# Optimization experiments

Measured on AMD Instinct MI355X. Metric: run time of the kernel, lower is better.

Reference implementation:

```python
import jax, jax.numpy as jnp
import numpy as np

NUM_HEADS = 16
HEAD_DIM = 64
D_MODEL = NUM_HEADS * HEAD_DIM  # 1024
B, L = 512, 64


def setup_inputs() -> dict:
    key = jax.random.key(0)
    ks = jax.random.split(key, 6)
    s = 1.0 / np.sqrt(D_MODEL)
    x = jax.random.normal(ks[0], (B, L, D_MODEL), dtype=jnp.float32)
    bias = jax.random.normal(ks[1], (1, NUM_HEADS, L, L), dtype=jnp.float32)
    Wq = jax.random.normal(ks[2], (D_MODEL, NUM_HEADS * HEAD_DIM), dtype=jnp.float32) * s
    Wk = jax.random.normal(ks[3], (D_MODEL, NUM_HEADS * HEAD_DIM), dtype=jnp.float32) * s
    Wv = jax.random.normal(ks[4], (D_MODEL, NUM_HEADS * HEAD_DIM), dtype=jnp.float32) * s
    Wo = jax.random.normal(ks[5], (NUM_HEADS * HEAD_DIM, D_MODEL), dtype=jnp.float32) * s
    return {"x": x, "bias": bias, "Wq": Wq, "Wk": Wk, "Wv": Wv, "Wo": Wo}


def reference(x, bias, Wq, Wk, Wv, Wo):
    Bsz, Ls, D = x.shape
    H, Dh = NUM_HEADS, HEAD_DIM
    # QKV projections (no bias), reshape to [B, H, L, Dh]
    q = (x @ Wq).reshape(Bsz, Ls, H, Dh).transpose(0, 2, 1, 3)
    k = (x @ Wk).reshape(Bsz, Ls, H, Dh).transpose(0, 2, 1, 3)
    v = (x @ Wv).reshape(Bsz, Ls, H, Dh).transpose(0, 2, 1, 3)
    scale = jnp.sqrt(jnp.float32(Dh))
    # [B, H, L, L]
    attn_logits = jnp.einsum('bhqd,bhkd->bhqk', q, k) / scale + bias
    attn_weights = jax.nn.softmax(attn_logits, axis=-1)
    # weighted sum -> [B, L, H*Dh]
    out = jnp.einsum('bhqk,bhkd->bhqd', attn_weights, v)
    out = out.transpose(0, 2, 1, 3).reshape(Bsz, Ls, H * Dh)
    return out @ Wo
```

## Files before the change

### kernel.cpp

```cpp
#include <hip/hip_runtime.h>
#include <hip/hip_bf16.h>
#include <stdint.h>

__device__ inline float bf2f(ushort u) {
    union { uint32_t u; float f; } v; v.u = ((uint32_t)u) << 16; return v.f;
}
__device__ inline ushort f2bf(float f) {
    union { float f; uint32_t u; } v; v.f = f;
    uint32_t u = v.u;
    uint32_t r = (u + 0x7fffu + ((u >> 16) & 1u)) >> 16;
    return (ushort)r;
}
__device__ inline uint32_t pk2bf(uint32_t flo, uint32_t fhi) {
    uint32_t lo = (flo + 0x7fffu + ((flo >> 16) & 1u)) >> 16;
    uint32_t hi = (fhi + 0x7fffu + ((fhi >> 16) & 1u)) >> 16;
    return lo | (hi << 16);
}

typedef __attribute__((ext_vector_type(8))) short bf16x8;
typedef __attribute__((ext_vector_type(4))) float f32x4;

__device__ inline void gload_lds16(const ushort* g, ushort* l) {
    __builtin_amdgcn_global_load_lds(
        (const __attribute__((address_space(1))) void*)g,
        (__attribute__((address_space(3))) void*)l, 16, 0, 0);
}

__global__ void transpose1024(const float* __restrict__ Wq, const float* __restrict__ Wk,
                              const float* __restrict__ Wv, const float* __restrict__ Wo,
                              ushort* __restrict__ WqT, ushort* __restrict__ WkT,
                              ushort* __restrict__ WvT, ushort* __restrict__ WoT) {
    const float* in; ushort* out;
    switch (blockIdx.z) {
        case 0: in = Wq; out = WqT; break;
        case 1: in = Wk; out = WkT; break;
        case 2: in = Wv; out = WvT; break;
        default: in = Wo; out = WoT; break;
    }
    __shared__ ushort tile[64][65];
    const int t = threadIdx.x;
    const int c = t & 63, rq = t >> 6;
    const int bx = blockIdx.x * 64, by = blockIdx.y * 64;
#pragma unroll
    for (int i = 0; i < 16; ++i) {
        int r = i * 4 + rq;
        tile[r][c] = f2bf(in[(size_t)(by + r) * 1024 + bx + c]);
    }
    __syncthreads();
#pragma unroll
    for (int i = 0; i < 16; ++i) {
        int r = i * 4 + rq;
        out[(size_t)(bx + r) * 1024 + by + c] = tile[c][r];
    }
}

__global__ __launch_bounds__(256)
void cast_bf16(const float* __restrict__ in, ushort* __restrict__ out, size_t n8) {
    size_t i = (size_t)blockIdx.x * blockDim.x + threadIdx.x;
    const size_t stride = (size_t)gridDim.x * blockDim.x;
    for (; i < n8; i += stride) {
        const uint4 lo = *(const uint4*)&in[i * 8];
        const uint4 hi = *(const uint4*)&in[i * 8 + 4];
        uint4 o;
        o.x = pk2bf(lo.x, lo.y); o.y = pk2bf(lo.z, lo.w);
        o.z = pk2bf(hi.x, hi.y); o.w = pk2bf(hi.z, hi.w);
        *(uint4*)&out[i * 8] = o;
    }
}

template <bool C_F32>
__global__ __launch_bounds__(512, 2)
void gemm256(const ushort* __restrict__ A, int lda, const ushort* __restrict__ Bt,
             void* __restrict__ C_, int M, int N, int K, int cm, int cn) {
    __shared__ __attribute__((aligned(16))) ushort lds[65536];
    const int t = threadIdx.x;
    const int lane = t & 63, wave = t >> 6;
    const int wm = wave >> 2, wn = wave & 3;
    const int quad = lane >> 4, l16 = lane & 15;

    const int gx = N >> 8;
    const int wg0 = blockIdx.y * gridDim.x + blockIdx.x;
    const int xcd = wg0 & 7, loc = wg0 >> 3;
    const int ncx = gx / cn;
    const int crow = xcd / ncx, ccol = xcd % ncx;
    int mt, nt;
    if (cn <= cm) { nt = ccol * cn + loc % cn; mt = crow * cm + loc / cn; }
    else          { mt = crow * cm + loc % cm; nt = ccol * cn + loc / cm; }
    const int m0 = mt << 8, n0 = nt << 8;

    const f32x4 zero = {0.f, 0.f, 0.f, 0.f};
    f32x4 acc[8][4];
#pragma unroll
    for (int i = 0; i < 8; ++i)
#pragma unroll
        for (int j = 0; j < 4; ++j) acc[i][j] = zero;

    auto STAGE = [&](const ushort* __restrict__ src, int ldb, int rc0, int kcol,
                     int regio, int buf) {
        ushort* l = &lds[buf * 32768 + regio];
#pragma unroll
        for (int j = 0; j < 2; ++j) {
            const int g = j * 512 + t;
            const int r = g >> 2;
            const int cg = (((g & 3) ^ ((r >> 1) & 3)) * 8);
            gload_lds16(&src[(size_t)(rc0 + r) * ldb + kcol + cg],
                        &l[(j * 512 + wave * 64) * 8]);
        }
    };
    auto LOFF = [&](int R) { return R * 32 + (quad ^ ((R >> 1) & 3)) * 8; };

    const int NT = K >> 6;
    STAGE(A, lda, m0, 0, 0, 0);
    STAGE(Bt, K, n0, 0, 16384, 0);
    STAGE(A, lda, m0, 32, 8192, 0);
    STAGE(Bt, K, n0, 32, 24576, 0);
    asm volatile("s_waitcnt vmcnt(4)" ::: "memory");
    __builtin_amdgcn_s_barrier();

    int cur = 0;
    for (int kt = 0; kt < NT; ++kt) {
        const bool nx = kt + 1 < NT;
        const int kn = (kt + 1) << 6;
        const ushort* la0 = &lds[cur * 32768];
        const ushort* lb0 = &lds[cur * 32768 + 16384];
        const ushort* la1 = la0 + 8192;
        const ushort* lb1 = lb0 + 8192;
        bf16x8 af[4], bf[4];

#pragma unroll
        for (int i = 0; i < 4; ++i) {
            af[i] = *(const bf16x8*)&la0[LOFF(wm * 128 + i * 16 + l16)];
            bf[i] = *(const bf16x8*)&lb0[LOFF(wn * 64 + i * 16 + l16)];
        }
        if (nx) STAGE(A, lda, m0, kn, 0, cur ^ 1);
        __builtin_amdgcn_sched_barrier(0);
        __builtin_amdgcn_s_barrier();
        asm volatile("s_waitcnt lgkmcnt(0)" ::: "memory");
        __builtin_amdgcn_sched_barrier(0);
        __builtin_amdgcn_s_setprio(1);
#pragma unroll
        for (int i = 0; i < 4; ++i)
#pragma unroll
            for (int n = 0; n < 4; ++n)
                acc[i][n] = __builtin_amdgcn_mfma_f32_16x16x32_bf16(af[i], bf[n], acc[i][n], 0, 0, 0);
        __builtin_amdgcn_s_setprio(0);
        __builtin_amdgcn_sched_barrier(0);
        __builtin_amdgcn_s_barrier();

#pragma unroll
        for (int i = 0; i < 4; ++i)
            af[i] = *(const bf16x8*)&la0[LOFF(wm * 128 + (i + 4) * 16 + l16)];
        if (nx) STAGE(Bt, K, n0, kn, 16384, cur ^ 1);
        __builtin_amdgcn_sched_barrier(0);
        __builtin_amdgcn_s_barrier();
        asm volatile("s_waitcnt lgkmcnt(0)" ::: "memory");
        __builtin_amdgcn_sched_barrier(0);
        __builtin_amdgcn_s_setprio(1);
#pragma unroll
        for (int i = 0; i < 4; ++i)
#pragma unroll
            for (int n = 0; n < 4; ++n)
                acc[i + 4][n] = __builtin_amdgcn_mfma_f32_16x16x32_bf16(af[i], bf[n], acc[i + 4][n], 0, 0, 0);
        __builtin_amdgcn_s_setprio(0);
        if (nx) asm volatile("s_waitcnt vmcnt(4)" ::: "memory");
        else    asm volatile("s_waitcnt vmcnt(0)" ::: "memory");
        __builtin_amdgcn_sched_barrier(0);
        __builtin_amdgcn_s_barrier();

#pragma unroll
        for (int i = 0; i < 4; ++i) {
            af[i] = *(const bf16x8*)&la1[LOFF(wm * 128 + i * 16 + l16)];
            bf[i] = *(const bf16x8*)&lb1[LOFF(wn * 64 + i * 16 + l16)];
        }
        if (nx) STAGE(A, lda, m0, kn + 32, 8192, cur ^ 1);
        __builtin_amdgcn_sched_barrier(0);
        __builtin_amdgcn_s_barrier();
        asm volatile("s_waitcnt lgkmcnt(0)" ::: "memory");
        __builtin_amdgcn_sched_barrier(0);
        __builtin_amdgcn_s_setprio(1);
#pragma unroll
        for (int i = 0; i < 4; ++i)
#pragma unroll
            for (int n = 0; n < 4; ++n)
                acc[i][n] = __builtin_amdgcn_mfma_f32_16x16x32_bf16(af[i], bf[n], acc[i][n], 0, 0, 0);
        __builtin_amdgcn_s_setprio(0);
        __builtin_amdgcn_sched_barrier(0);
        __builtin_amdgcn_s_barrier();

#pragma unroll
        for (int i = 0; i < 4; ++i)
            af[i] = *(const bf16x8*)&la1[LOFF(wm * 128 + (i + 4) * 16 + l16)];
        if (nx) STAGE(Bt, K, n0, kn + 32, 24576, cur ^ 1);
        __builtin_amdgcn_sched_barrier(0);
        __builtin_amdgcn_s_barrier();
        asm volatile("s_waitcnt lgkmcnt(0)" ::: "memory");
        __builtin_amdgcn_sched_barrier(0);
        __builtin_amdgcn_s_setprio(1);
#pragma unroll
        for (int i = 0; i < 4; ++i)
#pragma unroll
            for (int n = 0; n < 4; ++n)
                acc[i + 4][n] = __builtin_amdgcn_mfma_f32_16x16x32_bf16(af[i], bf[n], acc[i + 4][n], 0, 0, 0);
        __builtin_amdgcn_s_setprio(0);
        if (nx) asm volatile("s_waitcnt vmcnt(4)" ::: "memory");
        __builtin_amdgcn_sched_barrier(0);
        __builtin_amdgcn_s_barrier();

        cur ^= 1;
    }

#pragma unroll
    for (int mt2 = 0; mt2 < 8; ++mt2)
#pragma unroll
        for (int nt2 = 0; nt2 < 4; ++nt2)
#pragma unroll
            for (int r4 = 0; r4 < 4; ++r4) {
                const int row = m0 + wm * 128 + mt2 * 16 + quad * 4 + r4;
                const int col = n0 + wn * 64 + nt2 * 16 + l16;
                if (C_F32) ((float*)C_)[(size_t)row * N + col] = acc[mt2][nt2][r4];
                else       ((ushort*)C_)[(size_t)row * N + col] = f2bf(acc[mt2][nt2][r4]);
            }
}

__global__ __launch_bounds__(256)
void attn_mfma(ushort* __restrict__ QK, const ushort* __restrict__ Vt,
               const float* __restrict__ bias, int CROWS) {
    const int t = threadIdx.x;
    const int lane = t & 63, wave = t >> 6;
    const int quad = lane >> 4, l16 = lane & 15;
    const int b = blockIdx.x >> 4, h = blockIdx.x & 15;
    const int SQK = 2048;
    const size_t qbase = (size_t)b * 64 * SQK + (size_t)h * 64;
    const size_t kbase = qbase + 1024;
    const size_t vbase = (size_t)(h * 64) * CROWS + (size_t)b * 64;

    __shared__ __attribute__((aligned(16))) ushort Pl[4 * 16 * 72];

    bf16x8 qf[2];
#pragma unroll
    for (int ks = 0; ks < 2; ++ks)
        qf[ks] = *(const bf16x8*)&QK[qbase + (size_t)(wave * 16 + l16) * SQK + ks * 32 + quad * 8];

    const f32x4 zero = {0.f, 0.f, 0.f, 0.f};
    f32x4 s[4];
#pragma unroll
    for (int nt = 0; nt < 4; ++nt) s[nt] = zero;
#pragma unroll
    for (int nt = 0; nt < 4; ++nt)
#pragma unroll
        for (int ks = 0; ks < 2; ++ks) {
            bf16x8 kf = *(const bf16x8*)&QK[kbase + (size_t)(nt * 16 + l16) * SQK + ks * 32 + quad * 8];
            s[nt] = __builtin_amdgcn_mfma_f32_16x16x32_bf16(qf[ks], kf, s[nt], 0, 0, 0);
        }

    const int q0 = wave * 16 + quad * 4;
    float p[4][4];
#pragma unroll
    for (int nt = 0; nt < 4; ++nt)
#pragma unroll
        for (int r4 = 0; r4 < 4; ++r4)
            p[nt][r4] = s[nt][r4] * 0.125f +
                        bias[(size_t)(h * 64 + q0 + r4) * 64 + nt * 16 + l16];

    float rinv[4];
#pragma unroll
    for (int r4 = 0; r4 < 4; ++r4) {
        float m = fmaxf(fmaxf(p[0][r4], p[1][r4]), fmaxf(p[2][r4], p[3][r4]));
        m = fmaxf(m, __shfl_xor(m, 1));
        m = fmaxf(m, __shfl_xor(m, 2));
        m = fmaxf(m, __shfl_xor(m, 4));
        m = fmaxf(m, __shfl_xor(m, 8));
#pragma unroll
        for (int nt = 0; nt < 4; ++nt) p[nt][r4] = __expf(p[nt][r4] - m);
        float sum = p[0][r4] + p[1][r4] + p[2][r4] + p[3][r4];
        sum += __shfl_xor(sum, 1);
        sum += __shfl_xor(sum, 2);
        sum += __shfl_xor(sum, 4);
        sum += __shfl_xor(sum, 8);
        rinv[r4] = 1.f / sum;
    }

#pragma unroll
    for (int nt = 0; nt < 4; ++nt)
#pragma unroll
        for (int r4 = 0; r4 < 4; ++r4)
            Pl[(wave * 16 + quad * 4 + r4) * 72 + nt * 16 + l16] = f2bf(p[nt][r4]);
    __syncthreads();

    bf16x8 pa[2];
#pragma unroll
    for (int ks = 0; ks < 2; ++ks)
        pa[ks] = *(const bf16x8*)&Pl[(wave * 16 + l16) * 72 + ks * 32 + quad * 8];
    f32x4 o[4];
#pragma unroll
    for (int nt = 0; nt < 4; ++nt) o[nt] = zero;
#pragma unroll
    for (int nt = 0; nt < 4; ++nt)
#pragma unroll
        for (int ks = 0; ks < 2; ++ks) {
            bf16x8 vf = *(const bf16x8*)&Vt[vbase + (size_t)(nt * 16 + l16) * CROWS + ks * 32 + quad * 8];
            o[nt] = __builtin_amdgcn_mfma_f32_16x16x32_bf16(pa[ks], vf, o[nt], 0, 0, 0);
        }

#pragma unroll
    for (int nt = 0; nt < 4; ++nt)
#pragma unroll
        for (int r4 = 0; r4 < 4; ++r4)
            QK[qbase + (size_t)(q0 + r4) * SQK + nt * 16 + l16] = f2bf(o[nt][r4] * rinv[r4]);
}

extern "C" void kernel_launch(void* const* d_in, const int* in_sizes, int n_in,
                              void* d_out, int out_size, void* d_ws, size_t ws_size,
                              hipStream_t stream) {
    const float* x    = (const float*)d_in[0];
    const float* bias = (const float*)d_in[1];
    const float* Wq   = (const float*)d_in[2];
    const float* Wk   = (const float*)d_in[3];
    const float* Wv   = (const float*)d_in[4];
    const float* Wo   = (const float*)d_in[5];
    float* out = (float*)d_out;

    const size_t D = 1024;
    const size_t WB = 4 * D * D * 2;

    int CHUNK_B = 128;
    if (ws_size >= WB + (size_t)512 * 64 * 6144)      CHUNK_B = 512;
    else if (ws_size >= WB + (size_t)256 * 64 * 6144) CHUNK_B = 256;
    const int NCHUNK = 512 / CHUNK_B;
    const size_t CROWS = (size_t)CHUNK_B * 64;
    const size_t CELEM = CROWS * D;

    ushort* WqT = (ushort*)d_ws;
    ushort* WkT = WqT + D * D;
    ushort* WvT = WkT + D * D;
    ushort* WoT = WvT + D * D;
    ushort* QKc = WoT + D * D;
    ushort* Vtc = QKc + CROWS * 2048;

    transpose1024<<<dim3(16, 16, 4), 256, 0, stream>>>(Wq, Wk, Wv, Wo, WqT, WkT, WvT, WoT);

    for (int c = 0; c < NCHUNK; ++c) {
        const float* xc = x + (size_t)c * CELEM;
        float* outc = out + (size_t)c * CELEM;
        ushort* Xc = (ushort*)outc;
        cast_bf16<<<2048, 256, 0, stream>>>(xc, Xc, CELEM / 8);
        gemm256<false><<<dim3(8, CROWS / 256), 512, 0, stream>>>(
            Xc, 1024, WqT, QKc, (int)CROWS, 2048, 1024,
            (int)(CROWS / 256 / 4), 4);
        gemm256<false><<<dim3(CROWS / 256, 4), 512, 0, stream>>>(
            WvT, 1024, Xc, Vtc, 1024, (int)CROWS, 1024,
            4, (int)(CROWS / 256 / 8));
        attn_mfma<<<CHUNK_B * 16, 256, 0, stream>>>(QKc, Vtc, bias, (int)CROWS);
        gemm256<true><<<dim3(4, CROWS / 256), 512, 0, stream>>>(
            QKc, 2048, WoT, outc, (int)CROWS, 1024, 1024,
            (int)(CROWS / 256 / 4), 2);
    }
}
```

Measured before the change: 617.4 us.

## Make GEMM kernel persistent over consecutive tiles with cross-tile prefetch

The GEMM kernel now loops over T consecutive output tiles per workgroup, with a grid sized to 256 workgroups. It prefetches the next tile's first K slab during the current tile's last iteration and writes the epilogue inline. This hides the per-tile prologue and launch tail, but it drops the XCD-aware tile swizzle. That can hurt L2 locality, because consecutive tiles in a row-major walk share A rows but use different B columns.

Measured after the change: 649.2 us. +5.1%, slower.

```diff
diff --git a/kernel.cpp b/kernel.cpp
--- a/kernel.cpp
+++ b/kernel.cpp
@@ -71,22 +71,14 @@
 template <bool C_F32>
 __global__ __launch_bounds__(512, 2)
 void gemm256(const ushort* __restrict__ A, int lda, const ushort* __restrict__ Bt,
-             void* __restrict__ C_, int M, int N, int K, int cm, int cn) {
+             void* __restrict__ C_, int M, int N, int K, int T) {
     __shared__ __attribute__((aligned(16))) ushort lds[65536];
     const int t = threadIdx.x;
     const int lane = t & 63, wave = t >> 6;
     const int wm = wave >> 2, wn = wave & 3;
     const int quad = lane >> 4, l16 = lane & 15;
-
     const int gx = N >> 8;
-    const int wg0 = blockIdx.y * gridDim.x + blockIdx.x;
-    const int xcd = wg0 & 7, loc = wg0 >> 3;
-    const int ncx = gx / cn;
-    const int crow = xcd / ncx, ccol = xcd % ncx;
-    int mt, nt;
-    if (cn <= cm) { nt = ccol * cn + loc % cn; mt = crow * cm + loc / cn; }
-    else          { mt = crow * cm + loc % cm; nt = ccol * cn + loc / cm; }
-    const int m0 = mt << 8, n0 = nt << 8;
+    const int wg = blockIdx.x;
 
     const f32x4 zero = {0.f, 0.f, 0.f, 0.f};
     f32x4 acc[8][4];
@@ -110,17 +102,27 @@
     auto LOFF = [&](int R) { return R * 32 + (quad ^ ((R >> 1) & 3)) * 8; };
 
     const int NT = K >> 6;
-    STAGE(A, lda, m0, 0, 0, 0);
-    STAGE(Bt, K, n0, 0, 16384, 0);
-    STAGE(A, lda, m0, 32, 8192, 0);
-    STAGE(Bt, K, n0, 32, 24576, 0);
+    const int GEND = T * NT;
+
+    int tidc = wg * T;
+    int mC = (tidc / gx) << 8, nC = (tidc % gx) << 8;
+
+    STAGE(A, lda, mC, 0, 0, 0);
+    STAGE(Bt, K, nC, 0, 16384, 0);
+    STAGE(A, lda, mC, 32, 8192, 0);
+    STAGE(Bt, K, nC, 32, 24576, 0);
     asm volatile("s_waitcnt vmcnt(4)" ::: "memory");
     __builtin_amdgcn_s_barrier();
 
     int cur = 0;
-    for (int kt = 0; kt < NT; ++kt) {
-        const bool nx = kt + 1 < NT;
-        const int kn = (kt + 1) << 6;
+    for (int g = 0; g < GEND; ++g) {
+        const bool nx = g + 1 < GEND;
+        const int i2 = (g + 1) / NT, kt2 = (g + 1) - i2 * NT;
+        const int tidS = wg * T + i2;
+        const int mS = ((tidS / gx) << 8), nS = ((tidS % gx) << 8);
+        const int kS = kt2 << 6;
+        const bool tb = (kt2 == 0);
+
         const ushort* la0 = &lds[cur * 32768];
         const ushort* lb0 = &lds[cur * 32768 + 16384];
         const ushort* la1 = la0 + 8192;
@@ -132,7 +134,7 @@
             af[i] = *(const bf16x8*)&la0[LOFF(wm * 128 + i * 16 + l16)];
             bf[i] = *(const bf16x8*)&lb0[LOFF(wn * 64 + i * 16 + l16)];
         }
-        if (nx) STAGE(A, lda, m0, kn, 0, cur ^ 1);
+        if (nx) STAGE(A, lda, mS, kS, 0, cur ^ 1);
         __builtin_amdgcn_sched_barrier(0);
         __builtin_amdgcn_s_barrier();
         asm volatile("s_waitcnt lgkmcnt(0)" ::: "memory");
@@ -150,7 +152,7 @@
 #pragma unroll
         for (int i = 0; i < 4; ++i)
             af[i] = *(const bf16x8*)&la0[LOFF(wm * 128 + (i + 4) * 16 + l16)];
-        if (nx) STAGE(Bt, K, n0, kn, 16384, cur ^ 1);
+        if (nx) STAGE(Bt, K, nS, kS, 16384, cur ^ 1);
         __builtin_amdgcn_sched_barrier(0);
         __builtin_amdgcn_s_barrier();
         asm volatile("s_waitcnt lgkmcnt(0)" ::: "memory");
@@ -172,7 +174,7 @@
             af[i] = *(const bf16x8*)&la1[LOFF(wm * 128 + i * 16 + l16)];
             bf[i] = *(const bf16x8*)&lb1[LOFF(wn * 64 + i * 16 + l16)];
         }
-        if (nx) STAGE(A, lda, m0, kn + 32, 8192, cur ^ 1);
+        if (nx) STAGE(A, lda, mS, kS + 32, 8192, cur ^ 1);
         __builtin_amdgcn_sched_barrier(0);
         __builtin_amdgcn_s_barrier();
         asm volatile("s_waitcnt lgkmcnt(0)" ::: "memory");
@@ -190,7 +192,7 @@
 #pragma unroll
         for (int i = 0; i < 4; ++i)
             af[i] = *(const bf16x8*)&la1[LOFF(wm * 128 + (i + 4) * 16 + l16)];
-        if (nx) STAGE(Bt, K, n0, kn + 32, 24576, cur ^ 1);
+        if (nx) STAGE(Bt, K, nS, kS + 32, 24576, cur ^ 1);
         __builtin_amdgcn_sched_barrier(0);
         __builtin_amdgcn_s_barrier();
         asm volatile("s_waitcnt lgkmcnt(0)" ::: "memory");
@@ -207,19 +209,26 @@
         __builtin_amdgcn_s_barrier();
 
         cur ^= 1;
-    }
-
-#pragma unroll
-    for (int mt2 = 0; mt2 < 8; ++mt2)
-#pragma unroll
-        for (int nt2 = 0; nt2 < 4; ++nt2)
-#pragma unroll
-            for (int r4 = 0; r4 < 4; ++r4) {
-                const int row = m0 + wm * 128 + mt2 * 16 + quad * 4 + r4;
-                const int col = n0 + wn * 64 + nt2 * 16 + l16;
-                if (C_F32) ((float*)C_)[(size_t)row * N + col] = acc[mt2][nt2][r4];
-                else       ((ushort*)C_)[(size_t)row * N + col] = f2bf(acc[mt2][nt2][r4]);
-            }
+
+        if (tb) {
+#pragma unroll
+            for (int mt2 = 0; mt2 < 8; ++mt2)
+#pragma unroll
+                for (int nt2 = 0; nt2 < 4; ++nt2)
+#pragma unroll
+                    for (int r4 = 0; r4 < 4; ++r4) {
+                        const int row = mC + wm * 128 + mt2 * 16 + quad * 4 + r4;
+                        const int col = nC + wn * 64 + nt2 * 16 + l16;
+                        if (C_F32) ((float*)C_)[(size_t)row * N + col] = acc[mt2][nt2][r4];
+                        else       ((ushort*)C_)[(size_t)row * N + col] = f2bf(acc[mt2][nt2][r4]);
+                    }
+#pragma unroll
+            for (int i = 0; i < 8; ++i)
+#pragma unroll
+                for (int j = 0; j < 4; ++j) acc[i][j] = zero;
+            mC = mS; nC = nS;
+        }
+    }
 }
 
 __global__ __launch_bounds__(256)
@@ -339,20 +348,29 @@
 
     transpose1024<<<dim3(16, 16, 4), 256, 0, stream>>>(Wq, Wk, Wv, Wo, WqT, WkT, WvT, WoT);
 
+    auto tilesT = [](int ntile) { return ntile >= 256 ? ntile / 256 : 1; };
+
     for (int c = 0; c < NCHUNK; ++c) {
         const float* xc = x + (size_t)c * CELEM;
         float* outc = out + (size_t)c * CELEM;
         ushort* Xc = (ushort*)outc;
         cast_bf16<<<2048, 256, 0, stream>>>(xc, Xc, CELEM / 8);
-        gemm256<false><<<dim3(8, CROWS / 256), 512, 0, stream>>>(
-            Xc, 1024, WqT, QKc, (int)CROWS, 2048, 1024,
-            (int)(CROWS / 256 / 4), 4);
-        gemm256<false><<<dim3(CROWS / 256, 4), 512, 0, stream>>>(
-            WvT, 1024, Xc, Vtc, 1024, (int)CROWS, 1024,
-            4, (int)(CROWS / 256 / 8));
+
+        {
+            const int ntile = (int)(CROWS / 256) * 8, T = tilesT(ntile);
+            gemm256<false><<<ntile / T, 512, 0, stream>>>(
+                Xc, 1024, WqT, QKc, (int)CROWS, 2048, 1024, T);
+        }
+        {
+            const int ntile = 4 * (int)(CROWS / 256), T = tilesT(ntile);
+            gemm256<false><<<ntile / T, 512, 0, stream>>>(
+                WvT, 1024, Xc, Vtc, 1024, (int)CROWS, 1024, T);
+        }
         attn_mfma<<<CHUNK_B * 16, 256, 0, stream>>>(QKc, Vtc, bias, (int)CROWS);
-        gemm256<true><<<dim3(4, CROWS / 256), 512, 0, stream>>>(
-            QKc, 2048, WoT, outc, (int)CROWS, 1024, 1024,
-            (int)(CROWS / 256 / 4), 2);
-    }
-}
+        {
+            const int ntile = (int)(CROWS / 256) * 4, T = tilesT(ntile);
+            gemm256<true><<<ntile / T, 512, 0, stream>>>(
+                QKc, 2048, WoT, outc, (int)CROWS, 1024, 1024, T);
+        }
+    }
+}
```
